# Performance work log

Measured on AMD Instinct MI355X. Metric: run time of the kernel, lower is better.

## Reference

```python
import jax, jax.numpy as jnp
import numpy as np
from jax import lax

EPS = 1e-5
N_WIRES, N_LAYERS = 4, 3
DIM = 2 ** N_WIRES  # 16

# Static CNOT permutations for control w, target w+1 (state @ CNOT => new[k] = old[k ^ (((k>>c)&1)<<t)])
_idx = np.arange(DIM)
CNOT_PERMS = [jnp.asarray(_idx ^ (((_idx >> w) & 1) << (w + 1))) for w in range(N_WIRES - 1)]


def conv3x3(x, w):
    # x: [B,1,H,W], w: [1,1,3,3], padding=1, no bias
    return lax.conv_general_dilated(x, w, (1, 1), 'SAME',
                                    dimension_numbers=('NCHW', 'OIHW', 'NCHW'))


def batchnorm_train(x, gamma, beta):
    # training-mode BN: batch statistics over (B,H,W), biased variance
    mean = jnp.mean(x, axis=(0, 2, 3), keepdims=True)
    var = jnp.var(x, axis=(0, 2, 3), keepdims=True)
    xn = (x - mean) * lax.rsqrt(var + EPS)
    return xn * gamma.reshape(1, -1, 1, 1) + beta.reshape(1, -1, 1, 1)


def residual_block(x, w1, g1, b1, w2, g2, b2):
    out = jax.nn.relu(batchnorm_train(conv3x3(x, w1), g1, b1))
    out = batchnorm_train(conv3x3(out, w2), g2, b2)
    return jax.nn.relu(out + x)


def quantum_feat4(theta):
    # Faithful to QuantumKernel: real state, each RZ scales by cos(theta/2)
    # (rz[0,0]==rz[1,1]==cos(theta/2)), CNOT is a bit-indexed permutation.
    # State is independent of the patch values (patch is never used).
    s = jnp.zeros(DIM, dtype=theta.dtype).at[0].set(1.0)
    for l in range(N_LAYERS):
        s = s * jnp.prod(jnp.cos(theta[l] / 2.0))  # 8 RZ scalings for this layer
        for w in range(N_WIRES - 1):
            s = s[CNOT_PERMS[w]]
    probs = s ** 2
    return probs[:4]


def setup_inputs() -> dict:
    key = jax.random.key(0)
    ks = jax.random.split(key, 12)
    B = 16384
    d = dict(
        x=jax.random.normal(ks[0], (B, 1, 28, 28), dtype=jnp.float32),
        theta=jax.random.normal(ks[1], (N_LAYERS, N_WIRES, 2), dtype=jnp.float32),
        r1_w1=jax.random.normal(ks[2], (1, 1, 3, 3), dtype=jnp.float32) * 0.3,
        r1_g1=jnp.ones((1,), jnp.float32), r1_b1=jnp.zeros((1,), jnp.float32),
        r1_w2=jax.random.normal(ks[3], (1, 1, 3, 3), dtype=jnp.float32) * 0.3,
        r1_g2=jnp.ones((1,), jnp.float32), r1_b2=jnp.zeros((1,), jnp.float32),
        r2_w1=jax.random.normal(ks[4], (1, 1, 3, 3), dtype=jnp.float32) * 0.3,
        r2_g1=jnp.ones((1,), jnp.float32), r2_b1=jnp.zeros((1,), jnp.float32),
        r2_w2=jax.random.normal(ks[5], (1, 1, 3, 3), dtype=jnp.float32) * 0.3,
        r2_g2=jnp.ones((1,), jnp.float32), r2_b2=jnp.zeros((1,), jnp.float32),
        fc_w=jax.random.normal(ks[6], (10, 784), dtype=jnp.float32) * 0.03,
        fc_b=jnp.zeros((10,), jnp.float32),
        alpha=jnp.asarray(0.5, dtype=jnp.float32),
    )
    return d


def reference(x, theta, r1_w1, r1_g1, r1_b1, r1_w2, r1_g2, r1_b2,
              r2_w1, r2_g1, r2_b1, r2_w2, r2_g2, r2_b2, fc_w, fc_b, alpha):
    B = x.shape[0]
    cls_feat = residual_block(x, r1_w1, r1_g1, r1_b1, r1_w2, r1_g2, r1_b2)
    cls_feat = residual_block(cls_feat, r2_w1, r2_g1, r2_b1, r2_w2, r2_g2, r2_b2)
    cls_flat = cls_feat.reshape(B, -1)  # [B, 784]

    # Quantum filter: kernel output ignores patch values, identical for all
    # 196 patches and all batch elements; cat along dim=1 -> tile the 4-vector.
    p4 = quantum_feat4(theta)                           # [4]
    q_feat = jnp.broadcast_to(jnp.tile(p4, 14 * 14), (B, 784))

    fused = alpha * cls_flat + (1.0 - alpha) * q_feat
    logits = fused @ fc_w.T + fc_b
    return jax.nn.log_softmax(logits, axis=-1)
```

## Files before the change

kernel.cpp:

```cpp
#include <hip/hip_runtime.h>
#include <hip/hip_fp16.h>
#include <math.h>

#define BATCH   16384
#define IMGPIX  784
#define NTOT    (BATCH * IMGPIX)
#define NSLOT   64
#define SLOTSTR 8
#define STAGE_DBL (NSLOT * SLOTSTR)
#define TROW 224
#define TGRP 6272
#define CONVBLK 3584

struct __align__(8) h4 { __half2 lo, hi; };
__device__ __forceinline__ h4 f4_to_h4(float4 v) {
    h4 r; r.lo = __floats2half2_rn(v.x, v.y); r.hi = __floats2half2_rn(v.z, v.w); return r;
}
__device__ __forceinline__ float4 h4_to_f4(h4 p) {
    float2 a = __half22float2(p.lo), b = __half22float2(p.hi);
    return make_float4(a.x, a.y, b.x, b.y);
}
#define ZERO4 make_float4(0.f, 0.f, 0.f, 0.f)

__device__ __forceinline__ void block_stats_atomic(double lsum, double lsq, double* slot) {
    __shared__ double red[4][2];
    #pragma unroll
    for (int off = 32; off >= 1; off >>= 1) {
        lsum += __shfl_down(lsum, off, 64);
        lsq  += __shfl_down(lsq,  off, 64);
    }
    const int lane = threadIdx.x & 63;
    const int w    = threadIdx.x >> 6;
    if (lane == 0) { red[w][0] = lsum; red[w][1] = lsq; }
    __syncthreads();
    if (threadIdx.x == 0) {
        double ts = (red[0][0] + red[1][0]) + (red[2][0] + red[3][0]);
        double tq = (red[0][1] + red[1][1]) + (red[2][1] + red[3][1]);
        atomicAdd(&slot[0], ts);
        atomicAdd(&slot[1], tq);
    }
}

__device__ __forceinline__ float2 stats_ab(const double* __restrict__ stats_in,
                                           float gamma, float beta) {
    int lane = threadIdx.x & 63;
    double s = stats_in[lane * SLOTSTR];
    double q = stats_in[lane * SLOTSTR + 1];
    #pragma unroll
    for (int off = 32; off >= 1; off >>= 1) {
        s += __shfl_down(s, off, 64);
        q += __shfl_down(q, off, 64);
    }
    s = __shfl(s, 0, 64);
    q = __shfl(q, 0, 64);
    const double INV_N = 1.0 / (double)NTOT;
    double mean = s * INV_N;
    double var  = q * INV_N - mean * mean;
    float rstd = 1.0f / sqrtf((float)var + 1e-5f);
    float a  = gamma * rstd;
    float bb = beta - (float)mean * a;
    return make_float2(a, bb);
}

__device__ __forceinline__ float4 hrow(float wl, float wc, float wr,
                                       float L, float4 v, float R) {
    float4 h;
    h.x = fmaf(wl, L,   fmaf(wc, v.x, wr * v.y));
    h.y = fmaf(wl, v.x, fmaf(wc, v.y, wr * v.z));
    h.z = fmaf(wl, v.y, fmaf(wc, v.z, wr * v.w));
    h.w = fmaf(wl, v.z, fmaf(wc, v.w, wr * R));
    return h;
}

__device__ __forceinline__ void emit_row(__half* dst, int r, float4 o, float mf,
                                         double& lsum, double& lsq, bool act) {
    if (act) *(h4*)(dst + r * TROW) = f4_to_h4(o);
    float s4 = (o.x + o.y) + (o.z + o.w);
    float q4 = fmaf(o.x, o.x, fmaf(o.y, o.y, fmaf(o.z, o.z, o.w * o.w)));
    lsum += (double)(mf * s4);
    lsq  += (double)(mf * q4);
}

#define LANE_SETUP()                                                          \
    const int t = threadIdx.x;                                                \
    const int lane = t & 63;                                                  \
    const int widx = t >> 6;                                                  \
    const int c4   = lane & 7;                                                \
    const bool act = (c4 < 7);                                                \
    const float mf = act ? 1.f : 0.f;                                         \
    const int c4c  = c4 < 7 ? c4 : 6;                                         \
    const int task = blockIdx.x * 4 + widx;                     \
    const int s    = task >> 11;                              \
    const int G    = task & 2047;                          \
    const int r0   = s * 4;                                                   \
    const int rtop = (r0 > 0)  ? (r0 - 1) : 0;                                \
    const int rbot = (r0 < 24) ? (r0 + 4) : 27;                               \
    const int i8   = lane >> 3;                                               \
    const int img  = G * 8 + i8;                                              \
    const size_t xbase = (size_t)img * IMGPIX + c4c * 4;                      \
    const size_t tbR   = (size_t)G * TGRP + c4c * 32 + i8 * 4;                \
    const size_t tbW   = (size_t)G * TGRP + c4  * 32 + i8 * 4;

#define CONV_STEP(k, v)                                                       \
    {                                                                         \
        float L = __shfl_up((v).w, 1, 64);  if (c4 == 0) L = 0.f;             \
        float R = __shfl_down((v).x, 1, 64); if (c4 == 6) R = 0.f;            \
        float4 h2 = hrow(w9[6], w9[7], w9[8], L, (v), R);                     \
        float4 h1 = hrow(w9[3], w9[4], w9[5], L, (v), R);                     \
        float4 h0 = hrow(w9[0], w9[1], w9[2], L, (v), R);                     \
        accA.x += h2.x; accA.y += h2.y; accA.z += h2.z; accA.w += h2.w;       \
        if ((k) >= 2) emit_row(dst, r0 + (k) - 2, accA, mf, lsum, lsq, act);  \
        accA.x = accB.x + h1.x; accA.y = accB.y + h1.y;                       \
        accA.z = accB.z + h1.z; accA.w = accB.w + h1.w;                       \
        accB = h0;                                                            \
    }

#define HALO_ZERO(k, v)                                                       \
    if ((k) == 0 && r0 == 0)  (v) = ZERO4;                                    \
    if ((k) == 5 && r0 == 24) (v) = ZERO4;

__global__ __launch_bounds__(256, 8) void k_conv_plain(const float* __restrict__ in,
        const float* __restrict__ w, __half* __restrict__ out,
        __half* __restrict__ x16_out, double* __restrict__ stats_out)
{
    LANE_SETUP();
    float w9[9];
    #pragma unroll
    for (int i = 0; i < 9; i++) w9[i] = w[i];
    const float* src = in + xbase;
    __half* dst  = out + tbW;
    __half* dstx = x16_out + tbW;

    float4 vb[6];
    vb[0] = *(const float4*)(src + rtop * 28);
    #pragma unroll
    for (int k = 1; k < 5; k++) vb[k] = *(const float4*)(src + (r0 - 1 + k) * 28);
    vb[5] = *(const float4*)(src + rbot * 28);
    __builtin_amdgcn_sched_barrier(0);

    float4 accA = ZERO4, accB = ZERO4;
    double lsum = 0.0, lsq = 0.0;
    #pragma unroll
    for (int k = 0; k < 6; k++) {
        float4 v = vb[k];
        if (act && k >= 1 && k <= 4)
            *(h4*)(dstx + (r0 - 1 + k) * TROW) = f4_to_h4(vb[k]);
        HALO_ZERO(k, v);
        CONV_STEP(k, v);
    }
    block_stats_atomic(lsum, lsq, &stats_out[(blockIdx.x & (NSLOT - 1)) * SLOTSTR]);
}

__global__ __launch_bounds__(256, 8) void k_conv_affine(const __half* __restrict__ in,
        const double* __restrict__ stats_in,
        const float* __restrict__ gamma, const float* __restrict__ beta,
        const float* __restrict__ w, __half* __restrict__ out, double* __restrict__ stats_out)
{
    LANE_SETUP();
    float2 ab = stats_ab(stats_in, gamma[0], beta[0]);
    float w9[9];
    #pragma unroll
    for (int i = 0; i < 9; i++) w9[i] = w[i];
    const __half* src = in + tbR;
    __half* dst = out + tbW;

    h4 vb[6];
    vb[0] = *(const h4*)(src + rtop * TROW);
    #pragma unroll
    for (int k = 1; k < 5; k++) vb[k] = *(const h4*)(src + (r0 - 1 + k) * TROW);
    vb[5] = *(const h4*)(src + rbot * TROW);
    __builtin_amdgcn_sched_barrier(0);

    float4 accA = ZERO4, accB = ZERO4;
    double lsum = 0.0, lsq = 0.0;
    #pragma unroll
    for (int k = 0; k < 6; k++) {
        float4 r4 = h4_to_f4(vb[k]);
        float4 v;
        v.x = fmaxf(fmaf(ab.x, r4.x, ab.y), 0.f);
        v.y = fmaxf(fmaf(ab.x, r4.y, ab.y), 0.f);
        v.z = fmaxf(fmaf(ab.x, r4.z, ab.y), 0.f);
        v.w = fmaxf(fmaf(ab.x, r4.w, ab.y), 0.f);
        HALO_ZERO(k, v);
        CONV_STEP(k, v);
    }
    block_stats_atomic(lsum, lsq, &stats_out[(blockIdx.x & (NSLOT - 1)) * SLOTSTR]);
}

__global__ __launch_bounds__(256, 8) void k_conv_resid(const __half* __restrict__ y2,
        const __half* __restrict__ x16, const double* __restrict__ stats_in,
        const float* __restrict__ gamma, const float* __restrict__ beta,
        const float* __restrict__ w, __half* __restrict__ y3_out,
        __half* __restrict__ o1_out, double* __restrict__ stats_out)
{
    LANE_SETUP();
    float2 ab = stats_ab(stats_in, gamma[0], beta[0]);
    float w9[9];
    #pragma unroll
    for (int i = 0; i < 9; i++) w9[i] = w[i];
    const __half* srcy = y2 + tbR;
    const __half* srcx = x16 + tbR;
    __half* dst  = y3_out + tbW;
    __half* dsto = o1_out + tbW;

    h4 yb[6], xb[6];
    yb[0] = *(const h4*)(srcy + rtop * TROW);
    xb[0] = *(const h4*)(srcx + rtop * TROW);
    #pragma unroll
    for (int k = 1; k < 5; k++) {
        yb[k] = *(const h4*)(srcy + (r0 - 1 + k) * TROW);
        xb[k] = *(const h4*)(srcx + (r0 - 1 + k) * TROW);
    }
    yb[5] = *(const h4*)(srcy + rbot * TROW);
    xb[5] = *(const h4*)(srcx + rbot * TROW);
    __builtin_amdgcn_sched_barrier(0);

    float4 accA = ZERO4, accB = ZERO4;
    double lsum = 0.0, lsq = 0.0;
    #pragma unroll
    for (int k = 0; k < 6; k++) {
        float4 r4 = h4_to_f4(yb[k]);
        float4 x4 = h4_to_f4(xb[k]);
        float4 v;
        v.x = fmaxf(fmaf(ab.x, r4.x, ab.y) + x4.x, 0.f);
        v.y = fmaxf(fmaf(ab.x, r4.y, ab.y) + x4.y, 0.f);
        v.z = fmaxf(fmaf(ab.x, r4.z, ab.y) + x4.z, 0.f);
        v.w = fmaxf(fmaf(ab.x, r4.w, ab.y) + x4.w, 0.f);
        HALO_ZERO(k, v);
        if (act && k >= 1 && k <= 4)
            *(h4*)(dsto + (r0 - 1 + k) * TROW) = f4_to_h4(v);
        CONV_STEP(k, v);
    }
    block_stats_atomic(lsum, lsq, &stats_out[(blockIdx.x & (NSLOT - 1)) * SLOTSTR]);
}

__global__ __launch_bounds__(512, 4) void k_head(const __half* __restrict__ y4,
        const __half* __restrict__ o1, const double* __restrict__ stats_in,
        const float* __restrict__ gamma, const float* __restrict__ beta,
        const float* __restrict__ fc_w, const float* __restrict__ fc_b,
        const float* __restrict__ theta, const float* __restrict__ alpha_p,
        float* __restrict__ out)
{
    __shared__ float fcK[7840];
    __shared__ float accs[2][4][8][10];
    __shared__ float qk_s[10];
    const int t = threadIdx.x;
    float2 ab = stats_ab(stats_in, gamma[0], beta[0]);
    #pragma unroll
    for (int idx = t; idx < 7840; idx += 512) fcK[idx] = fc_w[idx];
    __syncthreads();
    if (t < 80) {
        int k = t >> 3, oct = t & 7;
        float s = 0.f;
        #pragma unroll
        for (int i = 0; i < 25; i++) {
            int p = oct + 8 * i;
            if (p < 196) s += fcK[k * 784 + p * 4];
        }
        s += __shfl_xor(s, 1, 64);
        s += __shfl_xor(s, 2, 64);
        s += __shfl_xor(s, 4, 64);
        if (oct == 0) {
            float c = 1.f;
            #pragma unroll
            for (int i = 0; i < 24; i++) c *= cosf(theta[i] * 0.5f);
            qk_s[k] = fmaf((1.f - alpha_p[0]) * c * c, s, fc_b[k]);
        }
    }
    __syncthreads();

    const int lane = t & 63;
    const int widx = t >> 6;
    const int Gloc = widx >> 2;
    const int q    = widx & 3;
    const int c4   = lane & 7;
    const int i8   = lane >> 3;
    const int c4c  = c4 < 7 ? c4 : 6;
    const float mf = (c4 < 7) ? 1.f : 0.f;
    const int G    = blockIdx.x * 2 + Gloc;
    const size_t tb = (size_t)G * TGRP + c4c * 32 + i8 * 4;
    const __half* ya = y4 + tb;
    const __half* oa = o1 + tb;

    float acc[10];
    #pragma unroll
    for (int k = 0; k < 10; k++) acc[k] = 0.f;

    #pragma unroll
    for (int rr = 0; rr < 7; rr++) {
        const int r = q * 7 + rr;
        float4 yf = h4_to_f4(*(const h4*)(ya + r * TROW));
        float4 of = h4_to_f4(*(const h4*)(oa + r * TROW));
        float4 v;
        v.x = fmaxf(fmaf(ab.x, yf.x, ab.y) + of.x, 0.f);
        v.y = fmaxf(fmaf(ab.x, yf.y, ab.y) + of.y, 0.f);
        v.z = fmaxf(fmaf(ab.x, yf.z, ab.y) + of.z, 0.f);
        v.w = fmaxf(fmaf(ab.x, yf.w, ab.y) + of.w, 0.f);
        const float* fb = &fcK[r * 28 + c4c * 4];
        #pragma unroll 5
        for (int k = 0; k < 10; k++) {
            const float4 f = *(const float4*)(fb + k * 784);
            acc[k] = fmaf(v.x, f.x, fmaf(v.y, f.y, fmaf(v.z, f.z, fmaf(v.w, f.w, acc[k]))));
        }
    }
    #pragma unroll
    for (int k = 0; k < 10; k++) {
        acc[k] *= mf;
        acc[k] += __shfl_xor(acc[k], 1, 64);
        acc[k] += __shfl_xor(acc[k], 2, 64);
        acc[k] += __shfl_xor(acc[k], 4, 64);
    }
    if (c4 == 0) {
        #pragma unroll
        for (int k = 0; k < 10; k++) accs[Gloc][q][i8][k] = acc[k];
    }
    __syncthreads();
    if (t < 16) {
        const int Gi = t >> 3, ii = t & 7;
        const float alpha = alpha_p[0];
        float l[10];
        float m = -1e30f;
        #pragma unroll
        for (int k = 0; k < 10; k++) {
            float ssum = (accs[Gi][0][ii][k] + accs[Gi][1][ii][k])
                       + (accs[Gi][2][ii][k] + accs[Gi][3][ii][k]);
            l[k] = fmaf(alpha, ssum, qk_s[k]);
            m = fmaxf(m, l[k]);
        }
        float se = 0.f;
        #pragma unroll
        for (int k = 0; k < 10; k++) se += __expf(l[k] - m);
        float lse = m + __logf(se);
        int img = (blockIdx.x * 2 + Gi) * 8 + ii;
        #pragma unroll
        for (int k = 0; k < 10; k++) out[(size_t)img * 10 + k] = l[k] - lse;
    }
}

extern "C" void kernel_launch(void* const* d_in, const int* in_sizes, int n_in,
                              void* d_out, int out_size, void* d_ws, size_t ws_size,
                              hipStream_t stream) {
    const float* x     = (const float*)d_in[0];
    const float* theta = (const float*)d_in[1];
    const float* r1_w1 = (const float*)d_in[2];
    const float* r1_g1 = (const float*)d_in[3];
    const float* r1_b1 = (const float*)d_in[4];
    const float* r1_w2 = (const float*)d_in[5];
    const float* r1_g2 = (const float*)d_in[6];
    const float* r1_b2 = (const float*)d_in[7];
    const float* r2_w1 = (const float*)d_in[8];
    const float* r2_g1 = (const float*)d_in[9];
    const float* r2_b1 = (const float*)d_in[10];
    const float* r2_w2 = (const float*)d_in[11];
    const float* r2_g2 = (const float*)d_in[12];
    const float* r2_b2 = (const float*)d_in[13];
    const float* fc_w  = (const float*)d_in[14];
    const float* fc_b  = (const float*)d_in[15];
    const float* alpha = (const float*)d_in[16];
    float* out = (float*)d_out;

    double* stats = (double*)d_ws;
    __half* bufA  = (__half*)((char*)d_ws + 32768);
    __half* bufB  = bufA + (size_t)NTOT;
    __half* bufD  = bufB + (size_t)NTOT;
    __half* bufX  = bufD + (size_t)NTOT;

    double* s_y1 = stats + 0 * STAGE_DBL;
    double* s_y2 = stats + 1 * STAGE_DBL;
    double* s_y3 = stats + 2 * STAGE_DBL;
    double* s_y4 = stats + 3 * STAGE_DBL;

    hipMemsetAsync(stats, 0, 4 * STAGE_DBL * sizeof(double), stream);
    k_conv_plain<<<CONVBLK, 256, 0, stream>>>(x, r1_w1, bufA, bufX, s_y1);
    k_conv_affine<<<CONVBLK, 256, 0, stream>>>(bufA, s_y1, r1_g1, r1_b1, r1_w2, bufB, s_y2);
    k_conv_resid<<<CONVBLK, 256, 0, stream>>>(bufB, bufX, s_y2, r1_g2, r1_b2, r2_w1, bufA, bufD, s_y3);
    k_conv_affine<<<CONVBLK, 256, 0, stream>>>(bufA, s_y3, r2_g1, r2_b1, r2_w2, bufB, s_y4);
    k_head<<<1024, 512, 0, stream>>>(bufB, bufD, s_y4, r2_g2, r2_b2,
                                     fc_w, fc_b, theta, alpha, out);
}
```

Before: 107.6 us.

## Use MFMA for FC head and prepack fp16 weights in extra conv block

New measurement: 109.3 us (median of 2 runs). No clear change (+1.7%).

```diff
diff --git a/kernel.cpp b/kernel.cpp
--- a/kernel.cpp
+++ b/kernel.cpp
@@ -11,6 +11,9 @@
 #define TROW 224
 #define TGRP 6272
 #define CONVBLK 3584
+
+typedef _Float16 half8 __attribute__((ext_vector_type(8)));
+typedef float f32x4 __attribute__((ext_vector_type(4)));
 
 struct __align__(8) h4 { __half2 lo, hi; };
 __device__ __forceinline__ h4 f4_to_h4(float4 v) {
@@ -121,8 +124,51 @@
 
 __global__ __launch_bounds__(256, 8) void k_conv_plain(const float* __restrict__ in,
         const float* __restrict__ w, __half* __restrict__ out,
-        __half* __restrict__ x16_out, double* __restrict__ stats_out)
+        __half* __restrict__ x16_out, double* __restrict__ stats_out,
+        const float* __restrict__ fc_w, const float* __restrict__ fc_b,
+        const float* __restrict__ theta, const float* __restrict__ alpha_p,
+        __half* __restrict__ Bpack, float* __restrict__ qkpad)
 {
+    if (blockIdx.x == CONVBLK) {
+        const int t = threadIdx.x;
+        for (int idx = t; idx < 28 * 512; idx += 256) {
+            int r = idx >> 9;
+            int l = (idx >> 3) & 63;
+            int j = idx & 7;
+            int n = l & 15;
+            int c = ((l >> 4) << 3) + j;
+            float v = 0.f;
+            if (c < 28 && n < 10) v = fc_w[n * 784 + r * 28 + c];
+            Bpack[idx] = __float2half(v);
+        }
+        __shared__ float csum[10];
+        if (t < 80) {
+            int k = t >> 3, oct = t & 7;
+            float s = 0.f;
+            #pragma unroll
+            for (int i = 0; i < 25; i++) {
+                int p = oct + 8 * i;
+                if (p < 196) s += fc_w[k * 784 + p * 4];
+            }
+            s += __shfl_xor(s, 1, 64);
+            s += __shfl_xor(s, 2, 64);
+            s += __shfl_xor(s, 4, 64);
+            if (oct == 0) csum[k] = s;
+        }
+        __syncthreads();
+        if (t < 16) {
+            float val = -1e30f;
+            if (t < 10) {
+                float c = 1.f;
+                #pragma unroll
+                for (int i = 0; i < 24; i++) c *= cosf(theta[i] * 0.5f);
+                val = fmaf((1.f - alpha_p[0]) * c * c, csum[t], fc_b[t]);
+            }
+            qkpad[t] = val;
+        }
+        return;
+    }
+
     LANE_SETUP();
     float w9[9];
     #pragma unroll
@@ -234,106 +280,86 @@
     block_stats_atomic(lsum, lsq, &stats_out[(blockIdx.x & (NSLOT - 1)) * SLOTSTR]);
 }
 
-__global__ __launch_bounds__(512, 4) void k_head(const __half* __restrict__ y4,
+__global__ __launch_bounds__(256, 4) void k_head_mfma(const __half* __restrict__ y4,
         const __half* __restrict__ o1, const double* __restrict__ stats_in,
         const float* __restrict__ gamma, const float* __restrict__ beta,
-        const float* __restrict__ fc_w, const float* __restrict__ fc_b,
-        const float* __restrict__ theta, const float* __restrict__ alpha_p,
-        float* __restrict__ out)
+        const __half* __restrict__ Bpack, const float* __restrict__ qkpad,
+        const float* __restrict__ alpha_p, float* __restrict__ out)
 {
-    __shared__ float fcK[7840];
-    __shared__ float accs[2][4][8][10];
-    __shared__ float qk_s[10];
-    const int t = threadIdx.x;
+    __shared__ float accs[4][64][4];
+    const int t    = threadIdx.x;
+    const int lane = t & 63;
+    const int q    = t >> 6;
     float2 ab = stats_ab(stats_in, gamma[0], beta[0]);
-    #pragma unroll
-    for (int idx = t; idx < 7840; idx += 512) fcK[idx] = fc_w[idx];
+
+    const int m   = lane & 15;
+    const int jg  = lane >> 4;
+    const int c4a = jg * 2;
+    const int c4b = (jg == 3) ? 6 : (jg * 2 + 1);
+    const int G   = blockIdx.x * 2 + (m >> 3);
+    const int i8  = m & 7;
+    const size_t base = (size_t)G * TGRP + i8 * 4;
+    const __half* ya = y4 + base;
+    const __half* oa = o1 + base;
+
+    f32x4 acc = {0.f, 0.f, 0.f, 0.f};
+    #pragma unroll
+    for (int rr = 0; rr < 7; rr++) {
+        const int r  = q * 7 + rr;
+        const int ro = r * TROW;
+        h4 ylo = *(const h4*)(ya + ro + c4a * 32);
+        h4 yhi = *(const h4*)(ya + ro + c4b * 32);
+        h4 olo = *(const h4*)(oa + ro + c4a * 32);
+        h4 ohi = *(const h4*)(oa + ro + c4b * 32);
+        float4 yf0 = h4_to_f4(ylo), yf1 = h4_to_f4(yhi);
+        float4 of0 = h4_to_f4(olo), of1 = h4_to_f4(ohi);
+        float4 va, vb;
+        va.x = fmaxf(fmaf(ab.x, yf0.x, ab.y) + of0.x, 0.f);
+        va.y = fmaxf(fmaf(ab.x, yf0.y, ab.y) + of0.y, 0.f);
+        va.z = fmaxf(fmaf(ab.x, yf0.z, ab.y) + of0.z, 0.f);
+        va.w = fmaxf(fmaf(ab.x, yf0.w, ab.y) + of0.w, 0.f);
+        vb.x = fmaxf(fmaf(ab.x, yf1.x, ab.y) + of1.x, 0.f);
+        vb.y = fmaxf(fmaf(ab.x, yf1.y, ab.y) + of1.y, 0.f);
+        vb.z = fmaxf(fmaf(ab.x, yf1.z, ab.y) + of1.z, 0.f);
+        vb.w = fmaxf(fmaf(ab.x, yf1.w, ab.y) + of1.w, 0.f);
+        union { half8 v; h4 qq[2]; } A;
+        A.qq[0] = f4_to_h4(va);
+        A.qq[1] = f4_to_h4(vb);
+        half8 B = *(const half8*)(Bpack + (r * 64 + lane) * 8);
+        acc = __builtin_amdgcn_mfma_f32_16x16x32_f16(A.v, B, acc, 0, 0, 0);
+    }
+    #pragma unroll
+    for (int i = 0; i < 4; i++) accs[q][lane][i] = acc[i];
     __syncthreads();
-    if (t < 80) {
-        int k = t >> 3, oct = t & 7;
-        float s = 0.f;
+
+    if (t < 64) {
+        float c[4];
         #pragma unroll
-        for (int i = 0; i < 25; i++) {
-            int p = oct + 8 * i;
-            if (p < 196) s += fcK[k * 784 + p * 4];
+        for (int i = 0; i < 4; i++)
+            c[i] = (accs[0][lane][i] + accs[1][lane][i])
+                 + (accs[2][lane][i] + accs[3][lane][i]);
+        const float alpha = alpha_p[0];
+        const int cls = lane & 15;
+        const float qv = qkpad[cls];
+        #pragma unroll
+        for (int i = 0; i < 4; i++) {
+            float logit = fmaf(alpha, c[i], qv);
+            float mx = logit;
+            mx = fmaxf(mx, __shfl_xor(mx, 1, 64));
+            mx = fmaxf(mx, __shfl_xor(mx, 2, 64));
+            mx = fmaxf(mx, __shfl_xor(mx, 4, 64));
+            mx = fmaxf(mx, __shfl_xor(mx, 8, 64));
+            float se = __expf(logit - mx);
+            se += __shfl_xor(se, 1, 64);
+            se += __shfl_xor(se, 2, 64);
+            se += __shfl_xor(se, 4, 64);
+            se += __shfl_xor(se, 8, 64);
+            float lse = mx + __logf(se);
+            if (cls < 10) {
+                int img = blockIdx.x * 16 + (lane >> 4) * 4 + i;
+                out[(size_t)img * 10 + cls] = logit - lse;
+            }
         }
-        s += __shfl_xor(s, 1, 64);
-        s += __shfl_xor(s, 2, 64);
-        s += __shfl_xor(s, 4, 64);
-        if (oct == 0) {
-            float c = 1.f;
-            #pragma unroll
-            for (int i = 0; i < 24; i++) c *= cosf(theta[i] * 0.5f);
-            qk_s[k] = fmaf((1.f - alpha_p[0]) * c * c, s, fc_b[k]);
-        }
-    }
-    __syncthreads();
-
-    const int lane = t & 63;
-    const int widx = t >> 6;
-    const int Gloc = widx >> 2;
-    const int q    = widx & 3;
-    const int c4   = lane & 7;
-    const int i8   = lane >> 3;
-    const int c4c  = c4 < 7 ? c4 : 6;
-    const float mf = (c4 < 7) ? 1.f : 0.f;
-    const int G    = blockIdx.x * 2 + Gloc;
-    const size_t tb = (size_t)G * TGRP + c4c * 32 + i8 * 4;
-    const __half* ya = y4 + tb;
-    const __half* oa = o1 + tb;
-
-    float acc[10];
-    #pragma unroll
-    for (int k = 0; k < 10; k++) acc[k] = 0.f;
-
-    #pragma unroll
-    for (int rr = 0; rr < 7; rr++) {
-        const int r = q * 7 + rr;
-        float4 yf = h4_to_f4(*(const h4*)(ya + r * TROW));
-        float4 of = h4_to_f4(*(const h4*)(oa + r * TROW));
-        float4 v;
-        v.x = fmaxf(fmaf(ab.x, yf.x, ab.y) + of.x, 0.f);
-        v.y = fmaxf(fmaf(ab.x, yf.y, ab.y) + of.y, 0.f);
-        v.z = fmaxf(fmaf(ab.x, yf.z, ab.y) + of.z, 0.f);
-        v.w = fmaxf(fmaf(ab.x, yf.w, ab.y) + of.w, 0.f);
-        const float* fb = &fcK[r * 28 + c4c * 4];
-        #pragma unroll 5
-        for (int k = 0; k < 10; k++) {
-            const float4 f = *(const float4*)(fb + k * 784);
-            acc[k] = fmaf(v.x, f.x, fmaf(v.y, f.y, fmaf(v.z, f.z, fmaf(v.w, f.w, acc[k]))));
-        }
-    }
-    #pragma unroll
-    for (int k = 0; k < 10; k++) {
-        acc[k] *= mf;
-        acc[k] += __shfl_xor(acc[k], 1, 64);
-        acc[k] += __shfl_xor(acc[k], 2, 64);
-        acc[k] += __shfl_xor(acc[k], 4, 64);
-    }
-    if (c4 == 0) {
-        #pragma unroll
-        for (int k = 0; k < 10; k++) accs[Gloc][q][i8][k] = acc[k];
-    }
-    __syncthreads();
-    if (t < 16) {
-        const int Gi = t >> 3, ii = t & 7;
-        const float alpha = alpha_p[0];
-        float l[10];
-        float m = -1e30f;
-        #pragma unroll
-        for (int k = 0; k < 10; k++) {
-            float ssum = (accs[Gi][0][ii][k] + accs[Gi][1][ii][k])
-                       + (accs[Gi][2][ii][k] + accs[Gi][3][ii][k]);
-            l[k] = fmaf(alpha, ssum, qk_s[k]);
-            m = fmaxf(m, l[k]);
-        }
-        float se = 0.f;
-        #pragma unroll
-        for (int k = 0; k < 10; k++) se += __expf(l[k] - m);
-        float lse = m + __logf(se);
-        int img = (blockIdx.x * 2 + Gi) * 8 + ii;
-        #pragma unroll
-        for (int k = 0; k < 10; k++) out[(size_t)img * 10 + k] = l[k] - lse;
     }
 }
 
@@ -360,7 +386,9 @@
     float* out = (float*)d_out;
 
     double* stats = (double*)d_ws;
-    __half* bufA  = (__half*)((char*)d_ws + 32768);
+    float*  qkpad = (float*)((char*)d_ws + 16384);
+    __half* Bpack = (__half*)((char*)d_ws + 16448);
+    __half* bufA  = (__half*)((char*)d_ws + 65536);
     __half* bufB  = bufA + (size_t)NTOT;
     __half* bufD  = bufB + (size_t)NTOT;
     __half* bufX  = bufD + (size_t)NTOT;
@@ -371,10 +399,12 @@
     double* s_y4 = stats + 3 * STAGE_DBL;
 
     hipMemsetAsync(stats, 0, 4 * STAGE_DBL * sizeof(double), stream);
-    k_conv_plain<<<CONVBLK, 256, 0, stream>>>(x, r1_w1, bufA, bufX, s_y1);
+    k_conv_plain<<<CONVBLK + 1, 256, 0, stream>>>(x, r1_w1, bufA, bufX, s_y1,
+                                                  fc_w, fc_b, theta, alpha,
+                                                  Bpack, qkpad);
     k_conv_affine<<<CONVBLK, 256, 0, stream>>>(bufA, s_y1, r1_g1, r1_b1, r1_w2, bufB, s_y2);
     k_conv_resid<<<CONVBLK, 256, 0, stream>>>(bufB, bufX, s_y2, r1_g2, r1_b2, r2_w1, bufA, bufD, s_y3);
     k_conv_affine<<<CONVBLK, 256, 0, stream>>>(bufA, s_y3, r2_g1, r2_b1, r2_w2, bufB, s_y4);
-    k_head<<<1024, 512, 0, stream>>>(bufB, bufD, s_y4, r2_g2, r2_b2,
-                                     fc_w, fc_b, theta, alpha, out);
-}
+    k_head_mfma<<<1024, 256, 0, stream>>>(bufB, bufD, s_y4, r2_g2, r2_b2,
+                                          Bpack, qkpad, alpha, out);
+}
```
